# Kernel tuning notes

Measured on AMD Instinct MI355X. Metric: run time of the kernel, lower is better.

## Reference

```python
import jax, jax.numpy as jnp
import numpy as np
from jax import lax

EPS = 1e-5
NEG_SLOPE = 0.01

def setup_inputs() -> dict:
    key = jax.random.key(0)
    ks = jax.random.split(key, 9)
    B, Cin, Cout, D, H, W = 2, 32, 64, 20, 20, 20
    x = jax.random.normal(ks[0], (B, Cin, D, H, W), dtype=jnp.float32)
    conv_w = jax.random.normal(ks[1], (Cout, Cin, 3, 3, 3), dtype=jnp.float32) * 0.05
    conv_b = jnp.zeros((Cout,), dtype=jnp.float32)
    gamma = jnp.ones((Cout,), dtype=jnp.float32)
    beta = jnp.zeros((Cout,), dtype=jnp.float32)
    wq = jax.random.normal(ks[2], (Cout, Cout), dtype=jnp.float32) * 0.05
    bq = jnp.zeros((Cout,), dtype=jnp.float32)
    wk = jax.random.normal(ks[3], (Cout, Cout), dtype=jnp.float32) * 0.05
    bk = jnp.zeros((Cout,), dtype=jnp.float32)
    wv = jax.random.normal(ks[4], (Cout, Cout), dtype=jnp.float32) * 0.05
    bv = jnp.zeros((Cout,), dtype=jnp.float32)
    return {"x": x, "conv_w": conv_w, "conv_b": conv_b, "gamma": gamma,
            "beta": beta, "wq": wq, "bq": bq, "wk": wk, "bk": bk,
            "wv": wv, "bv": bv}

def reference(x, conv_w, conv_b, gamma, beta, wq, bq, wk, bk, wv, bv):
    # Conv3d k=3, stride=1, padding=1 (SAME)
    y = lax.conv_general_dilated(
        x, conv_w, window_strides=(1, 1, 1), padding='SAME',
        dimension_numbers=('NCDHW', 'OIDHW', 'NCDHW'))
    y = y + conv_b[None, :, None, None, None]
    # InstanceNorm3d: normalize over spatial dims per (batch, channel)
    mu = jnp.mean(y, axis=(2, 3, 4), keepdims=True)
    var = jnp.mean(jnp.square(y - mu), axis=(2, 3, 4), keepdims=True)
    y = (y - mu) * lax.rsqrt(var + EPS)
    y = y * gamma[None, :, None, None, None] + beta[None, :, None, None, None]
    # LeakyReLU
    y = jnp.where(y >= 0, y, NEG_SLOPE * y)
    # Attention: 1x1x1 convs -> flatten -> bmm softmax bmm (no scaling)
    B, C, D, H, W = y.shape
    N = D * H * W
    f = y.reshape(B, C, N)                                  # [B, C, N]
    q = jnp.einsum('oc,bcn->bon', wq, f) + bq[None, :, None]
    k = jnp.einsum('oc,bcn->bon', wk, f) + bk[None, :, None]
    v = jnp.einsum('oc,bcn->bon', wv, f) + bv[None, :, None]
    att = jax.nn.softmax(jnp.einsum('bcn,bcm->bnm', q, k), axis=-1)  # [B,N,N]
    out = jnp.einsum('bck,bqk->bcq', v, att)                # [B, C, N]
    return out.reshape(B, C, D, H, W)
```

## Files before the change

kernel.cpp:

```cpp
#include <hip/hip_runtime.h>
#include <math.h>

#define CIN   32
#define COUT  64
#define DD    20
#define PD    22
#define PSP   (PD*PD*PD)
#define NSP   8000
#define BB    2
#define EPSN  1e-5f
#define SLOPE 0.01f

#define NT     250
#define SPLITS 8
#define QUADS  63

#define COG 4
#define OG  8

typedef float  f32x16 __attribute__((ext_vector_type(16)));
typedef short  short8 __attribute__((ext_vector_type(8)));

__device__ __forceinline__ unsigned short f2bf_rne(float x) {
    unsigned u = __float_as_uint(x);
    unsigned r = (u + 0x7FFFu + ((u >> 16) & 1u)) >> 16;
    return (unsigned short)r;
}
__device__ __forceinline__ float bf2f(unsigned short h) {
    return __uint_as_float(((unsigned)h) << 16);
}
__device__ __forceinline__ short8 ld_frag(const unsigned short* p) {
    uint4 t = *reinterpret_cast<const uint4*>(p);
    return __builtin_bit_cast(short8, t);
}
__device__ __forceinline__ void gload_lds16(const void* gsrc, void* ldst) {
    typedef __attribute__((address_space(1))) const unsigned int GU;
    typedef __attribute__((address_space(3))) unsigned int LU;
    __builtin_amdgcn_global_load_lds((GU*)gsrc, (LU*)ldst, 16, 0, 0);
}

__global__ void pad_k(const float* __restrict__ x, float* __restrict__ xp) {
    int idx = blockIdx.x * blockDim.x + threadIdx.x;
    if (idx >= BB * CIN * PSP) return;
    int pw = idx % PD;
    int ph = (idx / PD) % PD;
    int pd = (idx / (PD * PD)) % PD;
    int bc = idx / PSP;
    float v = 0.f;
    if (pw >= 1 && pw <= DD && ph >= 1 && ph <= DD && pd >= 1 && pd <= DD)
        v = x[(size_t)bc * NSP + ((size_t)(pd - 1) * DD + (ph - 1)) * DD + (pw - 1)];
    xp[idx] = v;
}

__global__ __launch_bounds__(256) void conv3d_k(const float* __restrict__ xp,
                                                const float* __restrict__ w,
                                                const float* __restrict__ bias,
                                                float* __restrict__ y) {
    int blk = blockIdx.x;
    int vb  = blk & 31;
    int cg  = (blk >> 5) & 15;
    int b   = blk >> 9;
    int vox = vb * 256 + threadIdx.x;
    bool valid = vox < NSP;
    int v  = valid ? vox : 0;
    int w_ = v % DD;
    int h_ = (v / DD) % DD;
    int d_ = v / (DD * DD);
    int pvox = ((d_ + 1) * PD + (h_ + 1)) * PD + (w_ + 1);
    const float* xb = xp + (size_t)b * CIN * PSP + pvox;

    float acc[COG];
    #pragma unroll
    for (int j = 0; j < COG; ++j) acc[j] = 0.f;

    for (int ci = 0; ci < CIN; ++ci) {
        const float* xc = xb + (size_t)ci * PSP;
        float xv[27];
        #pragma unroll
        for (int kd = 0; kd < 3; ++kd)
            #pragma unroll
            for (int kh = 0; kh < 3; ++kh)
                #pragma unroll
                for (int kw = 0; kw < 3; ++kw)
                    xv[(kd * 3 + kh) * 3 + kw] =
                        xc[(kd - 1) * (PD * PD) + (kh - 1) * PD + (kw - 1)];
        #pragma unroll
        for (int j = 0; j < COG; ++j) {
            int co = cg * COG + j;
            const float* wr = w + ((size_t)co * CIN + ci) * 27;
            float a = acc[j];
            #pragma unroll
            for (int t = 0; t < 27; ++t) a += xv[t] * wr[t];
            acc[j] = a;
        }
    }
    if (valid) {
        #pragma unroll
        for (int j = 0; j < COG; ++j) {
            int co = cg * COG + j;
            y[((size_t)b * COUT + co) * NSP + vox] = acc[j] + bias[co];
        }
    }
}

__global__ void instnorm_part_k(const float* __restrict__ y, float2* __restrict__ part) {
    int bc    = blockIdx.x >> 2;
    int chunk = blockIdx.x & 3;
    const float* yb = y + (size_t)bc * NSP + chunk * 2000;
    float s = 0.f, ss = 0.f;
    for (int i = threadIdx.x; i < 2000; i += 256) {
        float v = yb[i];
        s += v; ss += v * v;
    }
    __shared__ float rs[256], rss[256];
    rs[threadIdx.x] = s; rss[threadIdx.x] = ss;
    __syncthreads();
    for (int off = 128; off > 0; off >>= 1) {
        if (threadIdx.x < off) {
            rs[threadIdx.x]  += rs[threadIdx.x + off];
            rss[threadIdx.x] += rss[threadIdx.x + off];
        }
        __syncthreads();
    }
    if (threadIdx.x == 0) part[blockIdx.x] = make_float2(rs[0], rss[0]);
}

__global__ __launch_bounds__(256) void qkv_k(const float* __restrict__ yraw,
                      const float2* __restrict__ part,
                      const float* __restrict__ gamma, const float* __restrict__ beta,
                      const float* __restrict__ wq, const float* __restrict__ bq,
                      const float* __restrict__ wk, const float* __restrict__ bk,
                      const float* __restrict__ wv, const float* __restrict__ bv,
                      unsigned short* __restrict__ Qfh, unsigned short* __restrict__ Qfl,
                      unsigned short* __restrict__ Kfh,
                      unsigned short* __restrict__ Vf) {
    int blk = blockIdx.x;
    int vb  = blk & 31;
    int og  = (blk >> 5) & 7;
    int b   = blk >> 8;
    int n   = vb * 256 + threadIdx.x;
    bool valid = n < NSP;
    int nn  = valid ? n : 0;
    const float* fb = yraw + (size_t)b * COUT * NSP + nn;

    __shared__ float smean[COUT], srstd[COUT];
    if (threadIdx.x < COUT) {
        int c = threadIdx.x;
        float s = 0.f, ss = 0.f;
        #pragma unroll
        for (int ch = 0; ch < 4; ++ch) {
            float2 p = part[(b * COUT + c) * 4 + ch];
            s += p.x; ss += p.y;
        }
        float mean = s * (1.f / NSP);
        smean[c] = mean;
        srstd[c] = rsqrtf(ss * (1.f / NSP) - mean * mean + EPSN);
    }
    __syncthreads();

    float aq[OG], ak[OG], av[OG];
    #pragma unroll
    for (int j = 0; j < OG; ++j) {
        int o = og * OG + j;
        aq[j] = bq[o]; ak[j] = bk[o]; av[j] = bv[o];
    }
    for (int c = 0; c < COUT; ++c) {
        float fc = (fb[(size_t)c * NSP] - smean[c]) * srstd[c] * gamma[c] + beta[c];
        fc = fc >= 0.f ? fc : SLOPE * fc;
        #pragma unroll
        for (int j = 0; j < OG; ++j) {
            int o = og * OG + j;
            aq[j] += wq[o * COUT + c] * fc;
            ak[j] += wk[o * COUT + c] * fc;
            av[j] += wv[o * COUT + c] * fc;
        }
    }
    if (!valid) return;

    int t  = n >> 5;
    int kk = n & 31;
    unsigned short qh[OG], ql[OG], kh[OG];
    #pragma unroll
    for (int j = 0; j < OG; ++j) {
        qh[j] = f2bf_rne(aq[j]); ql[j] = f2bf_rne(aq[j] - bf2f(qh[j]));
        kh[j] = f2bf_rne(ak[j]);
    }
    size_t qko = ((size_t)((b * NT + t) * 4 + (og >> 1)) * 2 + (og & 1)) * 256 + kk * 8;
    *reinterpret_cast<uint4*>(Qfh + qko) = *reinterpret_cast<const uint4*>(qh);
    *reinterpret_cast<uint4*>(Qfl + qko) = *reinterpret_cast<const uint4*>(ql);
    *reinterpret_cast<uint4*>(Kfh + qko) = *reinterpret_cast<const uint4*>(kh);
    {
        int Y = kk >> 4, hf = (kk >> 3) & 1, e = kk & 7;
        size_t vbase = ((size_t)((b * NT + t) * 2 + Y) * 2 + (og >> 2)) * 512
                     + hf * 256 + e;
        #pragma unroll
        for (int j = 0; j < OG; ++j)
            Vf[vbase + ((og & 3) * 8 + j) * 8] = f2bf_rne(av[j]);
    }
}

__global__ __launch_bounds__(256, 4) void attn_pass1_mfma(
        const unsigned short* __restrict__ Qfh, const unsigned short* __restrict__ Qfl,
        const unsigned short* __restrict__ Kfh,
        const unsigned short* __restrict__ Vf,
        float* __restrict__ pm, float* __restrict__ pl, float* __restrict__ pacc) {
    int bid   = blockIdx.x;
    int split = bid / (BB * QUADS);
    int rem   = bid % (BB * QUADS);
    int b     = rem / QUADS;
    int quad  = rem % QUADS;
    int wave  = threadIdx.x >> 6;
    int lane  = threadIdx.x & 63;
    int col   = lane & 31;
    int half  = lane >> 5;
    int qt    = quad * 4 + wave;
    bool qvalid = qt < NT;
    int qtc   = qvalid ? qt : NT - 1;
    int bNT   = b * NT;

    int tstart = (split * NT) / SPLITS;
    int tend   = ((split + 1) * NT) / SPLITS;
    int nkt    = tend - tstart;

    __shared__ __align__(16) char ldsbuf[3][8192];

    short8 qfh[4], qfl[4];
    {
        const unsigned short* qp  = Qfh + (size_t)(bNT + qtc) * 2048 + lane * 8;
        const unsigned short* qp2 = Qfl + (size_t)(bNT + qtc) * 2048 + lane * 8;
        #pragma unroll
        for (int c = 0; c < 4; ++c) {
            qfh[c] = ld_frag(qp  + c * 512);
            qfl[c] = ld_frag(qp2 + c * 512);
        }
    }

    int wo = wave * 1024;
    int go = wo + lane * 16;

    auto STAGE = [&](int bufi, int tg) {
        size_t tb = (size_t)(bNT + tg) * 2048;
        char* l = &ldsbuf[bufi][0];
        gload_lds16((const char*)(Kfh + tb) + go, l + wo);
        gload_lds16((const char*)(Vf  + tb) + go, l + 4096 + wo);
    };

    f32x16 oacc0 = {};
    f32x16 oacc1 = {};
    float m = -3e38f, lsum = 0.f;

    STAGE(0, tstart);
    STAGE(1, tstart + 1);

    for (int t = 0; t < nkt; ++t) {
        if (t == nkt - 1) { asm volatile("s_waitcnt vmcnt(0)" ::: "memory"); }
        else              { asm volatile("s_waitcnt vmcnt(2)" ::: "memory"); }
        __builtin_amdgcn_sched_barrier(0);
        __builtin_amdgcn_s_barrier();
        __builtin_amdgcn_sched_barrier(0);
        if (t + 2 < nkt) STAGE((t + 2) % 3, tstart + t + 2);

        const unsigned short* lk = (const unsigned short*)&ldsbuf[t % 3][0];
        const unsigned short* lv = (const unsigned short*)&ldsbuf[t % 3][4096];

        f32x16 s = {};
        __builtin_amdgcn_s_setprio(1);
        #pragma unroll
        for (int c = 0; c < 4; ++c) {
            short8 kfh = ld_frag(lk + c * 512 + lane * 8);
            s = __builtin_amdgcn_mfma_f32_32x32x16_bf16(kfh, qfh[c], s, 0, 0, 0);
            s = __builtin_amdgcn_mfma_f32_32x32x16_bf16(kfh, qfl[c], s, 0, 0, 0);
        }
        __builtin_amdgcn_s_setprio(0);

        float t8[8];
        #pragma unroll
        for (int r = 0; r < 8; ++r) t8[r] = fmaxf(s[r], s[r + 8]);
        float t4a = fmaxf(t8[0], t8[1]), t4b = fmaxf(t8[2], t8[3]);
        float t4c = fmaxf(t8[4], t8[5]), t4d = fmaxf(t8[6], t8[7]);
        float tmax = fmaxf(fmaxf(t4a, t4b), fmaxf(t4c, t4d));
        tmax = fmaxf(tmax, __shfl_xor(tmax, 32, 64));
        if (__any(tmax > m + 8.f)) {
            float newm  = fmaxf(m, tmax);
            float scale = __expf(m - newm);
            lsum *= scale;
            #pragma unroll
            for (int r = 0; r < 16; ++r) { oacc0[r] *= scale; oacc1[r] *= scale; }
            m = newm;
        }
        short8 pf0, pf1;
        float ls;
        {
            float p[8];
            #pragma unroll
            for (int r = 0; r < 8; ++r) p[r] = __expf(s[r] - m);
            ls = ((p[0] + p[1]) + (p[2] + p[3])) + ((p[4] + p[5]) + (p[6] + p[7]));
            unsigned W[4], X[4];
            #pragma unroll
            for (int j = 0; j < 4; ++j)
                asm("v_cvt_pk_bf16_f32 %0, %1, %2" : "=v"(W[j]) : "v"(p[2 * j]), "v"(p[2 * j + 1]));
            #pragma unroll
            for (int j = 0; j < 4; ++j) X[j] = (unsigned)__shfl_xor((int)W[j], 32, 64);
            uint4 u = half ? make_uint4(X[2], X[3], W[2], W[3])
                           : make_uint4(W[0], W[1], X[0], X[1]);
            pf0 = __builtin_bit_cast(short8, u);
        }
        {
            float p[8];
            #pragma unroll
            for (int r = 0; r < 8; ++r) p[r] = __expf(s[r + 8] - m);
            ls += ((p[0] + p[1]) + (p[2] + p[3])) + ((p[4] + p[5]) + (p[6] + p[7]));
            unsigned W[4], X[4];
            #pragma unroll
            for (int j = 0; j < 4; ++j)
                asm("v_cvt_pk_bf16_f32 %0, %1, %2" : "=v"(W[j]) : "v"(p[2 * j]), "v"(p[2 * j + 1]));
            #pragma unroll
            for (int j = 0; j < 4; ++j) X[j] = (unsigned)__shfl_xor((int)W[j], 32, 64);
            uint4 u = half ? make_uint4(X[2], X[3], W[2], W[3])
                           : make_uint4(W[0], W[1], X[0], X[1]);
            pf1 = __builtin_bit_cast(short8, u);
        }
        lsum += ls;
        {
            short8 v00 = ld_frag(lv + 0 * 512 + lane * 8);
            short8 v10 = ld_frag(lv + 1 * 512 + lane * 8);
            __builtin_amdgcn_s_setprio(1);
            oacc0 = __builtin_amdgcn_mfma_f32_32x32x16_bf16(v00, pf0, oacc0, 0, 0, 0);
            oacc1 = __builtin_amdgcn_mfma_f32_32x32x16_bf16(v10, pf0, oacc1, 0, 0, 0);
            __builtin_amdgcn_s_setprio(0);
            short8 v01 = ld_frag(lv + 2 * 512 + lane * 8);
            short8 v11 = ld_frag(lv + 3 * 512 + lane * 8);
            __builtin_amdgcn_s_setprio(1);
            oacc0 = __builtin_amdgcn_mfma_f32_32x32x16_bf16(v01, pf1, oacc0, 0, 0, 0);
            oacc1 = __builtin_amdgcn_mfma_f32_32x32x16_bf16(v11, pf1, oacc1, 0, 0, 0);
            __builtin_amdgcn_s_setprio(0);
        }
    }

    if (!qvalid) return;
    int q0 = qt * 32;
    float lfull = lsum + __shfl_xor(lsum, 32, 64);
    size_t base = (size_t)b * SPLITS + split;
    if (lane < 32) {
        pm[base * NSP + q0 + col] = m;
        pl[base * NSP + q0 + col] = lfull;
    }
    float* pa = pacc + base * (size_t)(COUT * NSP) + q0 + col;
    #pragma unroll
    for (int r = 0; r < 16; ++r) {
        int crow = (r & 3) + 8 * (r >> 2) + 4 * half;
        pa[(size_t)crow * NSP]        = oacc0[r];
        pa[(size_t)(crow + 32) * NSP] = oacc1[r];
    }
}

__global__ void attn_combine_k(const float* __restrict__ pm, const float* __restrict__ pl,
                               const float* __restrict__ pacc, float* __restrict__ out) {
    int idx = blockIdx.x * blockDim.x + threadIdx.x;
    if (idx >= BB * COUT * NSP) return;
    int n = idx % NSP;
    int c = (idx / NSP) % COUT;
    int b = idx / (NSP * COUT);
    float M = -1e30f;
    #pragma unroll
    for (int j = 0; j < SPLITS; ++j)
        M = fmaxf(M, pm[((size_t)b * SPLITS + j) * NSP + n]);
    float L = 0.f, O = 0.f;
    #pragma unroll
    for (int j = 0; j < SPLITS; ++j) {
        size_t base = (size_t)b * SPLITS + j;
        float wgt = __expf(pm[base * NSP + n] - M);
        L += pl[base * NSP + n] * wgt;
        O += pacc[(base * COUT + c) * NSP + n] * wgt;
    }
    out[idx] = O / L;
}

extern "C" void kernel_launch(void* const* d_in, const int* in_sizes, int n_in,
                              void* d_out, int out_size, void* d_ws, size_t ws_size,
                              hipStream_t stream) {
    const float* x      = (const float*)d_in[0];
    const float* conv_w = (const float*)d_in[1];
    const float* conv_b = (const float*)d_in[2];
    const float* gamma  = (const float*)d_in[3];
    const float* beta   = (const float*)d_in[4];
    const float* wq     = (const float*)d_in[5];
    const float* bq     = (const float*)d_in[6];
    const float* wk     = (const float*)d_in[7];
    const float* bk     = (const float*)d_in[8];
    const float* wv     = (const float*)d_in[9];
    const float* bv     = (const float*)d_in[10];
    float* out = (float*)d_out;

    const int ELEMS = BB * COUT * NSP;
    char* w8 = (char*)d_ws;
    float*  y    = (float*)w8;
    float2* part = (float2*)(w8 + 4096000);
    unsigned short* Qfh = (unsigned short*)(w8 + 4100096);
    unsigned short* Qfl = Qfh + (size_t)ELEMS;
    unsigned short* Kfh = Qfl + (size_t)ELEMS;
    unsigned short* Vf  = Kfh + (size_t)ELEMS;
    float* pm   = (float*)(Vf + (size_t)ELEMS);
    float* pl   = pm + (size_t)BB * SPLITS * NSP;
    float* pacc = pl + (size_t)BB * SPLITS * NSP;
    float* xpad = pacc;

    pad_k<<<(BB * CIN * PSP + 255) / 256, 256, 0, stream>>>(x, xpad);
    conv3d_k<<<BB * 16 * 32, 256, 0, stream>>>(xpad, conv_w, conv_b, y);
    instnorm_part_k<<<BB * COUT * 4, 256, 0, stream>>>(y, part);
    qkv_k<<<BB * 8 * 32, 256, 0, stream>>>(y, part, gamma, beta,
                                           wq, bq, wk, bk, wv, bv,
                                           Qfh, Qfl, Kfh, Vf);
    attn_pass1_mfma<<<SPLITS * BB * QUADS, 256, 0, stream>>>(Qfh, Qfl, Kfh, Vf,
                                                             pm, pl, pacc);
    attn_combine_k<<<(ELEMS + 255) / 256, 256, 0, stream>>>(pm, pl, pacc, out);
}
```

Before: 151.6 us.

## Fuse instance-norm statistics into conv and switch softmax to base-2 exp

Instance-norm partial sums are now computed inside the conv kernel with wave shuffles and an LDS reduce, which removes the separate instnorm_part kernel launch and the re-read of y. Q is pre-scaled by log2(e) so the attention softmax and the combine step can use raw v_exp_f32 (exp2) instead of __expf. The lazy-rescale threshold rises from 8 to 11.5 in log2 units, and the max reduction is restructured. The workspace offset is moved to fit the larger partial-sum buffer. Using exp2 with pre-scaled bf16 Q changes rounding slightly, and the looser threshold risks larger unnormalised values before a rescale.

```diff
diff --git a/kernel.cpp b/kernel.cpp
--- a/kernel.cpp
+++ b/kernel.cpp
@@ -10,6 +10,7 @@
 #define BB    2
 #define EPSN  1e-5f
 #define SLOPE 0.01f
+#define LOG2E 1.4426950408889634f
 
 #define NT     250
 #define SPLITS 8
@@ -37,6 +38,16 @@
     typedef __attribute__((address_space(1))) const unsigned int GU;
     typedef __attribute__((address_space(3))) unsigned int LU;
     __builtin_amdgcn_global_load_lds((GU*)gsrc, (LU*)ldst, 16, 0, 0);
+}
+__device__ __forceinline__ float exp2_fast(float x) {
+    float r;
+    asm("v_exp_f32 %0, %1" : "=v"(r) : "v"(x));
+    return r;
+}
+__device__ __forceinline__ float wsum(float x) {
+    #pragma unroll
+    for (int off = 1; off < 64; off <<= 1) x += __shfl_xor(x, off, 64);
+    return x;
 }
 
 __global__ void pad_k(const float* __restrict__ x, float* __restrict__ xp) {
@@ -55,7 +66,8 @@
 __global__ __launch_bounds__(256) void conv3d_k(const float* __restrict__ xp,
                                                 const float* __restrict__ w,
                                                 const float* __restrict__ bias,
-                                                float* __restrict__ y) {
+                                                float* __restrict__ y,
+                                                float2* __restrict__ part) {
     int blk = blockIdx.x;
     int vb  = blk & 31;
     int cg  = (blk >> 5) & 15;
@@ -94,35 +106,27 @@
             acc[j] = a;
         }
     }
-    if (valid) {
-        #pragma unroll
-        for (int j = 0; j < COG; ++j) {
-            int co = cg * COG + j;
-            y[((size_t)b * COUT + co) * NSP + vox] = acc[j] + bias[co];
-        }
-    }
-}
-
-__global__ void instnorm_part_k(const float* __restrict__ y, float2* __restrict__ part) {
-    int bc    = blockIdx.x >> 2;
-    int chunk = blockIdx.x & 3;
-    const float* yb = y + (size_t)bc * NSP + chunk * 2000;
-    float s = 0.f, ss = 0.f;
-    for (int i = threadIdx.x; i < 2000; i += 256) {
-        float v = yb[i];
-        s += v; ss += v * v;
-    }
-    __shared__ float rs[256], rss[256];
-    rs[threadIdx.x] = s; rss[threadIdx.x] = ss;
+
+    __shared__ float2 wred[4][COG];
+    int wv = threadIdx.x >> 6;
+    int ln = threadIdx.x & 63;
+    #pragma unroll
+    for (int j = 0; j < COG; ++j) {
+        int co = cg * COG + j;
+        float val = valid ? acc[j] + bias[co] : 0.f;
+        if (valid) y[((size_t)b * COUT + co) * NSP + vox] = val;
+        float s  = wsum(val);
+        float ss = wsum(val * val);
+        if (ln == 0) wred[wv][j] = make_float2(s, ss);
+    }
     __syncthreads();
-    for (int off = 128; off > 0; off >>= 1) {
-        if (threadIdx.x < off) {
-            rs[threadIdx.x]  += rs[threadIdx.x + off];
-            rss[threadIdx.x] += rss[threadIdx.x + off];
-        }
-        __syncthreads();
-    }
-    if (threadIdx.x == 0) part[blockIdx.x] = make_float2(rs[0], rss[0]);
+    if (threadIdx.x < COG) {
+        int j = threadIdx.x;
+        float s = 0.f, ss = 0.f;
+        #pragma unroll
+        for (int w2 = 0; w2 < 4; ++w2) { s += wred[w2][j].x; ss += wred[w2][j].y; }
+        part[((size_t)(b * COUT + cg * COG + j)) * 32 + vb] = make_float2(s, ss);
+    }
 }
 
 __global__ __launch_bounds__(256) void qkv_k(const float* __restrict__ yraw,
@@ -147,9 +151,9 @@
     if (threadIdx.x < COUT) {
         int c = threadIdx.x;
         float s = 0.f, ss = 0.f;
-        #pragma unroll
-        for (int ch = 0; ch < 4; ++ch) {
-            float2 p = part[(b * COUT + c) * 4 + ch];
+        #pragma unroll 8
+        for (int ch = 0; ch < 32; ++ch) {
+            float2 p = part[(size_t)(b * COUT + c) * 32 + ch];
             s += p.x; ss += p.y;
         }
         float mean = s * (1.f / NSP);
@@ -182,7 +186,8 @@
     unsigned short qh[OG], ql[OG], kh[OG];
     #pragma unroll
     for (int j = 0; j < OG; ++j) {
-        qh[j] = f2bf_rne(aq[j]); ql[j] = f2bf_rne(aq[j] - bf2f(qh[j]));
+        float q2 = aq[j] * LOG2E;
+        qh[j] = f2bf_rne(q2); ql[j] = f2bf_rne(q2 - bf2f(qh[j]));
         kh[j] = f2bf_rne(ak[j]);
     }
     size_t qko = ((size_t)((b * NT + t) * 4 + (og >> 1)) * 2 + (og & 1)) * 256 + kk * 8;
@@ -273,16 +278,16 @@
         }
         __builtin_amdgcn_s_setprio(0);
 
-        float t8[8];
-        #pragma unroll
-        for (int r = 0; r < 8; ++r) t8[r] = fmaxf(s[r], s[r + 8]);
-        float t4a = fmaxf(t8[0], t8[1]), t4b = fmaxf(t8[2], t8[3]);
-        float t4c = fmaxf(t8[4], t8[5]), t4d = fmaxf(t8[6], t8[7]);
-        float tmax = fmaxf(fmaxf(t4a, t4b), fmaxf(t4c, t4d));
+        float a0 = fmaxf(fmaxf(s[0],  s[1]),  s[2]);
+        float a1 = fmaxf(fmaxf(s[3],  s[4]),  s[5]);
+        float a2 = fmaxf(fmaxf(s[6],  s[7]),  s[8]);
+        float a3 = fmaxf(fmaxf(s[9],  s[10]), s[11]);
+        float a4 = fmaxf(fmaxf(s[12], s[13]), s[14]);
+        float tmax = fmaxf(fmaxf(fmaxf(a0, a1), a2), fmaxf(fmaxf(a3, a4), s[15]));
         tmax = fmaxf(tmax, __shfl_xor(tmax, 32, 64));
-        if (__any(tmax > m + 8.f)) {
+        if (__any(tmax > m + 11.5f)) {
             float newm  = fmaxf(m, tmax);
-            float scale = __expf(m - newm);
+            float scale = exp2_fast(m - newm);
             lsum *= scale;
             #pragma unroll
             for (int r = 0; r < 16; ++r) { oacc0[r] *= scale; oacc1[r] *= scale; }
@@ -293,7 +298,7 @@
         {
             float p[8];
             #pragma unroll
-            for (int r = 0; r < 8; ++r) p[r] = __expf(s[r] - m);
+            for (int r = 0; r < 8; ++r) p[r] = exp2_fast(s[r] - m);
             ls = ((p[0] + p[1]) + (p[2] + p[3])) + ((p[4] + p[5]) + (p[6] + p[7]));
             unsigned W[4], X[4];
             #pragma unroll
@@ -308,7 +313,7 @@
         {
             float p[8];
             #pragma unroll
-            for (int r = 0; r < 8; ++r) p[r] = __expf(s[r + 8] - m);
+            for (int r = 0; r < 8; ++r) p[r] = exp2_fast(s[r + 8] - m);
             ls += ((p[0] + p[1]) + (p[2] + p[3])) + ((p[4] + p[5]) + (p[6] + p[7]));
             unsigned W[4], X[4];
             #pragma unroll
@@ -369,7 +374,9 @@
     #pragma unroll
     for (int j = 0; j < SPLITS; ++j) {
         size_t base = (size_t)b * SPLITS + j;
-        float wgt = __expf(pm[base * NSP + n] - M);
+        float d = pm[base * NSP + n] - M;
+        float wgt;
+        asm("v_exp_f32 %0, %1" : "=v"(wgt) : "v"(d));
         L += pl[base * NSP + n] * wgt;
         O += pacc[(base * COUT + c) * NSP + n] * wgt;
     }
@@ -396,7 +403,7 @@
     char* w8 = (char*)d_ws;
     float*  y    = (float*)w8;
     float2* part = (float2*)(w8 + 4096000);
-    unsigned short* Qfh = (unsigned short*)(w8 + 4100096);
+    unsigned short* Qfh = (unsigned short*)(w8 + 4128768);
     unsigned short* Qfl = Qfh + (size_t)ELEMS;
     unsigned short* Kfh = Qfl + (size_t)ELEMS;
     unsigned short* Vf  = Kfh + (size_t)ELEMS;
@@ -406,8 +413,7 @@
     float* xpad = pacc;
 
     pad_k<<<(BB * CIN * PSP + 255) / 256, 256, 0, stream>>>(x, xpad);
-    conv3d_k<<<BB * 16 * 32, 256, 0, stream>>>(xpad, conv_w, conv_b, y);
-    instnorm_part_k<<<BB * COUT * 4, 256, 0, stream>>>(y, part);
+    conv3d_k<<<BB * 16 * 32, 256, 0, stream>>>(xpad, conv_w, conv_b, y, part);
     qkv_k<<<BB * 8 * 32, 256, 0, stream>>>(y, part, gamma, beta,
                                            wq, bq, wk, bk, wv, bv,
                                            Qfh, Qfl, Kfh, Vf);
```

Result: faster. 146.5 us (-3.4%).
